# Optimization experiments

Hardware: AMD Instinct MI355X
Metric: run time of the kernel (lower is better)

The kernel has to match this reference:

```python
import jax, jax.numpy as jnp
import numpy as np

# split_shape from init_kwargs: list of (K, L) = (num slices, slice length)
SPLITS = [(1, 400), (60, 256), (36, 256)]
D_MODEL = 512
BATCH = 2048
EPS = 1e-5  # torch LayerNorm default


def setup_inputs() -> dict:
    key = jax.random.key(0)
    n = len(SPLITS)
    ks = jax.random.split(key, 1 + n)
    total_dim = sum(k * l for k, l in SPLITS)
    inp = {"x": jax.random.normal(ks[0], (BATCH, total_dim), jnp.float32)}
    for i, (k, l) in enumerate(SPLITS):
        # orthogonal-ish init approximated by scaled normal; LN affine = identity
        inp[f"W{i}"] = jax.random.normal(ks[1 + i], (l, D_MODEL), jnp.float32) / np.sqrt(l).astype(np.float32)
        inp[f"b{i}"] = jnp.zeros((D_MODEL,), jnp.float32)
        inp[f"g{i}"] = jnp.ones((D_MODEL,), jnp.float32)
        inp[f"be{i}"] = jnp.zeros((D_MODEL,), jnp.float32)
    return inp


def _fc_block(xs, W, b, g, be):
    # xs: [B, K, L] -> Linear + ReLU + LayerNorm -> [B, K, D]
    h = jax.nn.relu(jnp.einsum('bkl,ld->bkd', xs, W) + b)
    mu = jnp.mean(h, axis=-1, keepdims=True)
    var = jnp.var(h, axis=-1, keepdims=True)
    return (h - mu) * jax.lax.rsqrt(var + EPS) * g + be


def reference(x, W0, b0, g0, be0, W1, b1, g1, be1, W2, b2, g2, be2):
    params = [(W0, b0, g0, be0), (W1, b1, g1, be1), (W2, b2, g2, be2)]
    outs = []
    start = 0
    B = x.shape[0]
    for (k, l), (W, b, g, be) in zip(SPLITS, params):
        # the torch loop over j (K slices) is one batched GEMM after a reshape
        seg = x[:, start:start + k * l].reshape(B, k, l)
        outs.append(_fc_block(seg, W, b, g, be))
        start += k * l
    # torch.stack(x1, 1) over all K_i slices == concat of per-split [B,K_i,D]
    return jnp.concatenate(outs, axis=1)  # [B, sum(K_i)=97, D]
```

## Files before the change

### kernel.cpp

```cpp
#include <hip/hip_runtime.h>

#define TOTAL_DIM 24976
#define N_ROWS    97
#define D_MODEL   512
#define EPSLN     1e-5f

#define NB0 32
#define NB1 1920
#define NB2 1152

#define WT_TOTAL 475136
#define WT_BYTES (WT_TOTAL * 2)

#define SMEM_FUSED 61952

typedef __attribute__((ext_vector_type(8))) short frag8;
typedef __attribute__((ext_vector_type(4))) float frag4;

__device__ __forceinline__ unsigned short f2b(float f) {
  unsigned u = __float_as_uint(f);
  u = u + 0x7fffu + ((u >> 16) & 1u);
  return (unsigned short)(u >> 16);
}

__device__ __forceinline__ unsigned cvt2bf(float lo, float hi) {
  unsigned r;
  asm("v_cvt_pk_bf16_f32 %0, %1, %2" : "=v"(r) : "v"(lo), "v"(hi));
  return r;
}

__global__ void __launch_bounds__(256) prep_wt(const float* __restrict__ W0,
                                               const float* __restrict__ W1,
                                               const float* __restrict__ W2,
                                               unsigned short* __restrict__ wt) {
  int i = blockIdx.x * 256 + threadIdx.x;
  if (i >= WT_TOTAL / 4) return;
  const float* W; int L, NSTEP, u;
  if (i < 53248)      { W = W0; L = 400; NSTEP = 13; u = i; }
  else if (i < 86016) { W = W1; L = 256; NSTEP = 8;  u = i - 53248; }
  else                { W = W2; L = 256; NSTEP = 8;  u = i - 86016; }
  int j4 = u & 1;
  int l  = (u >> 1) & 63;
  int fi = u >> 7;
  int t  = fi % NSTEP;
  int nt = fi / NSTEP;
  int n  = nt * 16 + (l & 15);
  int k0 = t * 32 + (l >> 4) * 8 + j4 * 4;
  float v[4];
#pragma unroll
  for (int j = 0; j < 4; ++j) {
    int k = k0 + j;
    v[j] = (k < L) ? W[k * 512 + n] : 0.f;
  }
  unsigned lo = (unsigned)f2b(v[0]) | ((unsigned)f2b(v[1]) << 16);
  unsigned hi = (unsigned)f2b(v[2]) | ((unsigned)f2b(v[3]) << 16);
  ((uint2*)wt)[i] = make_uint2(lo, hi);
}

template <int S>
__device__ __forceinline__ void run_split(
    int blk, char* smem,
    const float* __restrict__ x, const unsigned short* __restrict__ wt,
    const float* __restrict__ bias, const float* __restrict__ gam,
    const float* __restrict__ bet, float* __restrict__ out) {
  constexpr int L     = (S == 0) ? 400 : 256;
  constexpr int KP    = (S == 0) ? 416 : 256;
  constexpr int NSTEP = KP / 32;
  constexpr int START = (S == 0) ? 0 : (S == 1) ? 400 : 15760;
  constexpr int KK    = (S == 0) ? 1 : (S == 1) ? 60 : 36;
  constexpr int OFF   = (S == 0) ? 0 : (S == 1) ? 1 : 61;
  constexpr int WTO   = (S == 0) ? 0 : (S == 1) ? 212992 : 344064;
  constexpr int RS    = KP * 2;
  constexpr bool SWZ  = (S != 0);

  unsigned short* A = (unsigned short*)smem;
  float* red  = (float*)(smem + 64 * RS);
  float* stat = (float*)(smem + 64 * RS + 8192);

  const int tid  = threadIdx.x;
  const int lane = tid & 63, w = tid >> 6;
  const int q = lane >> 4, c = lane & 15;
  const int m_base = blk * 64;

  const unsigned short* bp0 = wt + WTO + (2 * w) * (NSTEP * 512) + lane * 8;
  const unsigned short* bp1 = bp0 + NSTEP * 512;

  frag8 bc0 = *(const frag8*)bp0;
  frag8 bc1 = *(const frag8*)bp1;

  {
    int r = tid >> 4, ch = tid & 15;
    int m = m_base + r;
    int bb = m / KK, jj = m - bb * KK;
    const float* rp = x + (size_t)bb * TOTAL_DIM + START + (size_t)jj * L;
    constexpr int NPASS = (S == 0) ? 7 : 4;
#pragma unroll
    for (int p = 0; p < NPASS; ++p) {
      int c4 = ch + p * 16;
      if (S == 0 && c4 >= 104) continue;
      float4 v;
      if (S == 0 && c4 >= 100) {
        v.x = 0.f; v.y = 0.f; v.z = 0.f; v.w = 0.f;
      } else {
        v = *(const float4*)(rp + c4 * 4);
      }
      unsigned lo = cvt2bf(v.x, v.y), hi = cvt2bf(v.z, v.w);
      int off = c4 * 8;
      if (SWZ) off ^= ((r & 7) << 4);
      *(uint2*)((char*)A + r * RS + off) = make_uint2(lo, hi);
    }
  }

  frag4 acc[4][2];
#pragma unroll
  for (int mt = 0; mt < 4; ++mt)
#pragma unroll
    for (int nt = 0; nt < 2; ++nt) {
      frag4 z = {0.f, 0.f, 0.f, 0.f};
      acc[mt][nt] = z;
    }

  __syncthreads();

  const int sw = SWZ ? ((c & 7) << 4) : 0;

#pragma unroll
  for (int t = 0; t < NSTEP; ++t) {
    frag8 bn0, bn1;
    const bool pre = (t + 1 < NSTEP);
    if (pre) {
      bn0 = *(const frag8*)(bp0 + (t + 1) * 512);
      bn1 = *(const frag8*)(bp1 + (t + 1) * 512);
    }
    frag8 af[4];
    const int off = (t * 64 + q * 16) ^ sw;
#pragma unroll
    for (int mt = 0; mt < 4; ++mt)
      af[mt] = *(const frag8*)((char*)A + (mt * 16 + c) * RS + off);
#pragma unroll
    for (int mt = 0; mt < 4; ++mt) {
      acc[mt][0] = __builtin_amdgcn_mfma_f32_16x16x32_bf16(af[mt], bc0, acc[mt][0], 0, 0, 0);
      acc[mt][1] = __builtin_amdgcn_mfma_f32_16x16x32_bf16(af[mt], bc1, acc[mt][1], 0, 0, 0);
    }
    if (pre) { bc0 = bn0; bc1 = bn1; }
  }

  const int colbase = w * 32 + c;
  float bv[2], gv[2], ev[2];
#pragma unroll
  for (int nt = 0; nt < 2; ++nt) {
    int col = colbase + nt * 16;
    bv[nt] = bias[col];
    gv[nt] = gam[col];
    ev[nt] = bet[col];
  }

#pragma unroll
  for (int mt = 0; mt < 4; ++mt) {
    float s[4] = {0.f, 0.f, 0.f, 0.f}, s2[4] = {0.f, 0.f, 0.f, 0.f};
#pragma unroll
    for (int nt = 0; nt < 2; ++nt)
#pragma unroll
      for (int r = 0; r < 4; ++r) {
        float h = acc[mt][nt][r] + bv[nt];
        h = fmaxf(h, 0.f);
        acc[mt][nt][r] = h;
        s[r] += h;
        s2[r] += h * h;
      }
#pragma unroll
    for (int r = 0; r < 4; ++r) {
      float a = s[r], b2 = s2[r];
#pragma unroll
      for (int msk = 1; msk < 16; msk <<= 1) {
        a += __shfl_xor(a, msk, 64);
        b2 += __shfl_xor(b2, msk, 64);
      }
      if (c == 0) {
        int row = mt * 16 + q * 4 + r;
        red[(w * 64 + row) * 2 + 0] = a;
        red[(w * 64 + row) * 2 + 1] = b2;
      }
    }
  }
  __syncthreads();
  if (tid < 64) {
    float s = 0.f, s2 = 0.f;
#pragma unroll
    for (int ww = 0; ww < 16; ++ww) {
      s  += red[(ww * 64 + tid) * 2 + 0];
      s2 += red[(ww * 64 + tid) * 2 + 1];
    }
    float mu  = s * (1.f / 512.f);
    float var = s2 * (1.f / 512.f) - mu * mu;
    stat[tid * 2 + 0] = mu;
    stat[tid * 2 + 1] = rsqrtf(var + EPSLN);
  }
  __syncthreads();

#pragma unroll
  for (int mt = 0; mt < 4; ++mt)
#pragma unroll
    for (int r = 0; r < 4; ++r) {
      int row = mt * 16 + q * 4 + r;
      float mu = stat[row * 2 + 0], sc = stat[row * 2 + 1];
      int m = m_base + row;
      int bb = m / KK, jj = m - bb * KK;
      size_t orow = (size_t)bb * N_ROWS + OFF + jj;
      float* op = out + orow * D_MODEL + colbase;
#pragma unroll
      for (int nt = 0; nt < 2; ++nt)
        op[nt * 16] = (acc[mt][nt][r] - mu) * sc * gv[nt] + ev[nt];
    }
}

__global__ void __launch_bounds__(1024, 4) fused_kernel(
    const float* __restrict__ x, const unsigned short* __restrict__ wt,
    const float* __restrict__ b0, const float* __restrict__ g0, const float* __restrict__ e0,
    const float* __restrict__ b1, const float* __restrict__ g1, const float* __restrict__ e1,
    const float* __restrict__ b2, const float* __restrict__ g2, const float* __restrict__ e2,
    float* __restrict__ out) {
  extern __shared__ char smem[];
  int bid = blockIdx.x;
  if (bid < NB0)
    run_split<0>(bid, smem, x, wt, b0, g0, e0, out);
  else if (bid < NB0 + NB1)
    run_split<1>(bid - NB0, smem, x, wt, b1, g1, e1, out);
  else
    run_split<2>(bid - NB0 - NB1, smem, x, wt, b2, g2, e2, out);
}

template <int S>
__global__ void __launch_bounds__(256) fallback_split(
    const float* __restrict__ x, const float* __restrict__ W,
    const float* __restrict__ bias, const float* __restrict__ gam,
    const float* __restrict__ bet, float* __restrict__ out) {
  constexpr int L     = (S == 0) ? 400 : 256;
  constexpr int START = (S == 0) ? 0 : (S == 1) ? 400 : 15760;
  constexpr int KK    = (S == 0) ? 1 : (S == 1) ? 60 : 36;
  constexpr int OFF   = (S == 0) ? 0 : (S == 1) ? 1 : 61;

  __shared__ float xs[400];
  __shared__ float rs[4], rs2[4];

  int m = blockIdx.x;
  int bb = m / KK, jj = m - bb * KK;
  const float* xp = x + (size_t)bb * TOTAL_DIM + START + jj * L;
  for (int k = threadIdx.x; k < L; k += 256) xs[k] = xp[k];
  __syncthreads();

  float h[2];
#pragma unroll
  for (int i = 0; i < 2; ++i) {
    int col = threadIdx.x + i * 256;
    float acc = 0.f;
    for (int k = 0; k < L; ++k) acc += xs[k] * W[k * 512 + col];
    h[i] = fmaxf(acc + bias[col], 0.f);
  }

  float s = h[0] + h[1], s2 = h[0] * h[0] + h[1] * h[1];
#pragma unroll
  for (int msk = 1; msk < 64; msk <<= 1) {
    s  += __shfl_xor(s, msk, 64);
    s2 += __shfl_xor(s2, msk, 64);
  }
  int wave = threadIdx.x >> 6, lane = threadIdx.x & 63;
  if (lane == 0) { rs[wave] = s; rs2[wave] = s2; }
  __syncthreads();
  s  = rs[0] + rs[1] + rs[2] + rs[3];
  s2 = rs2[0] + rs2[1] + rs2[2] + rs2[3];
  float mu  = s * (1.f / 512.f);
  float var = s2 * (1.f / 512.f) - mu * mu;
  float sc  = rsqrtf(var + EPSLN);

  float* op = out + ((size_t)bb * N_ROWS + OFF + jj) * D_MODEL;
#pragma unroll
  for (int i = 0; i < 2; ++i) {
    int col = threadIdx.x + i * 256;
    op[col] = (h[i] - mu) * sc * gam[col] + bet[col];
  }
}

extern "C" void kernel_launch(void* const* d_in, const int* in_sizes, int n_in,
                              void* d_out, int out_size, void* d_ws, size_t ws_size,
                              hipStream_t stream) {
  const float* x  = (const float*)d_in[0];
  const float* W0 = (const float*)d_in[1];
  const float* b0 = (const float*)d_in[2];
  const float* g0 = (const float*)d_in[3];
  const float* e0 = (const float*)d_in[4];
  const float* W1 = (const float*)d_in[5];
  const float* b1 = (const float*)d_in[6];
  const float* g1 = (const float*)d_in[7];
  const float* e1 = (const float*)d_in[8];
  const float* W2 = (const float*)d_in[9];
  const float* b2 = (const float*)d_in[10];
  const float* g2 = (const float*)d_in[11];
  const float* e2 = (const float*)d_in[12];
  float* out = (float*)d_out;

  if (ws_size >= (size_t)WT_BYTES) {
    unsigned short* wt = (unsigned short*)d_ws;
    prep_wt<<<464, 256, 0, stream>>>(W0, W1, W2, wt);
    fused_kernel<<<NB0 + NB1 + NB2, 1024, SMEM_FUSED, stream>>>(
        x, wt, b0, g0, e0, b1, g1, e1, b2, g2, e2, out);
  } else {
    fallback_split<0><<<2048,   256, 0, stream>>>(x, W0, b0, g0, e0, out);
    fallback_split<1><<<122880, 256, 0, stream>>>(x, W1, b1, g1, e1, out);
    fallback_split<2><<<73728,  256, 0, stream>>>(x, W2, b2, g2, e2, out);
  }
}
```

Baseline: 681.0 us.

## Switch to persistent 256-block kernel with register-resident weights and prefetched A tiles

Replaces the one-tile-per-block grid with 256 persistent blocks that each process 24 tiles of 32 rows. Each wave keeps its full weight slice in registers across tiles, and the next tile's x rows are prefetched into registers while the current tile's MFMAs run. Split 0 tiles are folded into the first 64 blocks of the split-2 range. The aim is to cut repeated weight loads and block launch overhead and to hide global latency. The cost is higher register pressure, a smaller M tile per block, and a fixed tile mapping hardcoded to this batch size.

```diff
diff --git a/kernel.cpp b/kernel.cpp
--- a/kernel.cpp
+++ b/kernel.cpp
@@ -5,14 +5,10 @@
 #define D_MODEL   512
 #define EPSLN     1e-5f
 
-#define NB0 32
-#define NB1 1920
-#define NB2 1152
-
 #define WT_TOTAL 475136
 #define WT_BYTES (WT_TOTAL * 2)
 
-#define SMEM_FUSED 61952
+#define SMEM_FUSED 30976
 
 typedef __attribute__((ext_vector_type(8))) short frag8;
 typedef __attribute__((ext_vector_type(4))) float frag4;
@@ -57,106 +53,13 @@
   ((uint2*)wt)[i] = make_uint2(lo, hi);
 }
 
-template <int S>
-__device__ __forceinline__ void run_split(
-    int blk, char* smem,
-    const float* __restrict__ x, const unsigned short* __restrict__ wt,
-    const float* __restrict__ bias, const float* __restrict__ gam,
-    const float* __restrict__ bet, float* __restrict__ out) {
-  constexpr int L     = (S == 0) ? 400 : 256;
-  constexpr int KP    = (S == 0) ? 416 : 256;
-  constexpr int NSTEP = KP / 32;
-  constexpr int START = (S == 0) ? 0 : (S == 1) ? 400 : 15760;
-  constexpr int KK    = (S == 0) ? 1 : (S == 1) ? 60 : 36;
-  constexpr int OFF   = (S == 0) ? 0 : (S == 1) ? 1 : 61;
-  constexpr int WTO   = (S == 0) ? 0 : (S == 1) ? 212992 : 344064;
-  constexpr int RS    = KP * 2;
-  constexpr bool SWZ  = (S != 0);
-
-  unsigned short* A = (unsigned short*)smem;
-  float* red  = (float*)(smem + 64 * RS);
-  float* stat = (float*)(smem + 64 * RS + 8192);
-
-  const int tid  = threadIdx.x;
-  const int lane = tid & 63, w = tid >> 6;
-  const int q = lane >> 4, c = lane & 15;
-  const int m_base = blk * 64;
-
-  const unsigned short* bp0 = wt + WTO + (2 * w) * (NSTEP * 512) + lane * 8;
-  const unsigned short* bp1 = bp0 + NSTEP * 512;
-
-  frag8 bc0 = *(const frag8*)bp0;
-  frag8 bc1 = *(const frag8*)bp1;
-
-  {
-    int r = tid >> 4, ch = tid & 15;
-    int m = m_base + r;
-    int bb = m / KK, jj = m - bb * KK;
-    const float* rp = x + (size_t)bb * TOTAL_DIM + START + (size_t)jj * L;
-    constexpr int NPASS = (S == 0) ? 7 : 4;
-#pragma unroll
-    for (int p = 0; p < NPASS; ++p) {
-      int c4 = ch + p * 16;
-      if (S == 0 && c4 >= 104) continue;
-      float4 v;
-      if (S == 0 && c4 >= 100) {
-        v.x = 0.f; v.y = 0.f; v.z = 0.f; v.w = 0.f;
-      } else {
-        v = *(const float4*)(rp + c4 * 4);
-      }
-      unsigned lo = cvt2bf(v.x, v.y), hi = cvt2bf(v.z, v.w);
-      int off = c4 * 8;
-      if (SWZ) off ^= ((r & 7) << 4);
-      *(uint2*)((char*)A + r * RS + off) = make_uint2(lo, hi);
-    }
-  }
-
-  frag4 acc[4][2];
-#pragma unroll
-  for (int mt = 0; mt < 4; ++mt)
-#pragma unroll
-    for (int nt = 0; nt < 2; ++nt) {
-      frag4 z = {0.f, 0.f, 0.f, 0.f};
-      acc[mt][nt] = z;
-    }
-
-  __syncthreads();
-
-  const int sw = SWZ ? ((c & 7) << 4) : 0;
-
-#pragma unroll
-  for (int t = 0; t < NSTEP; ++t) {
-    frag8 bn0, bn1;
-    const bool pre = (t + 1 < NSTEP);
-    if (pre) {
-      bn0 = *(const frag8*)(bp0 + (t + 1) * 512);
-      bn1 = *(const frag8*)(bp1 + (t + 1) * 512);
-    }
-    frag8 af[4];
-    const int off = (t * 64 + q * 16) ^ sw;
-#pragma unroll
-    for (int mt = 0; mt < 4; ++mt)
-      af[mt] = *(const frag8*)((char*)A + (mt * 16 + c) * RS + off);
-#pragma unroll
-    for (int mt = 0; mt < 4; ++mt) {
-      acc[mt][0] = __builtin_amdgcn_mfma_f32_16x16x32_bf16(af[mt], bc0, acc[mt][0], 0, 0, 0);
-      acc[mt][1] = __builtin_amdgcn_mfma_f32_16x16x32_bf16(af[mt], bc1, acc[mt][1], 0, 0, 0);
-    }
-    if (pre) { bc0 = bn0; bc1 = bn1; }
-  }
-
-  const int colbase = w * 32 + c;
-  float bv[2], gv[2], ev[2];
-#pragma unroll
-  for (int nt = 0; nt < 2; ++nt) {
-    int col = colbase + nt * 16;
-    bv[nt] = bias[col];
-    gv[nt] = gam[col];
-    ev[nt] = bet[col];
-  }
-
-#pragma unroll
-  for (int mt = 0; mt < 4; ++mt) {
+template <int KK, int OFF>
+__device__ __forceinline__ void epilogue32(
+    frag4 (&acc)[2][2], int m_base, int w, int q, int c, int tid, int colbase,
+    const float (&bv)[2], const float (&gv)[2], const float (&ev)[2],
+    float* red, float* stat, float* __restrict__ out) {
+#pragma unroll
+  for (int mt = 0; mt < 2; ++mt) {
     float s[4] = {0.f, 0.f, 0.f, 0.f}, s2[4] = {0.f, 0.f, 0.f, 0.f};
 #pragma unroll
     for (int nt = 0; nt < 2; ++nt)
@@ -178,18 +81,18 @@
       }
       if (c == 0) {
         int row = mt * 16 + q * 4 + r;
-        red[(w * 64 + row) * 2 + 0] = a;
-        red[(w * 64 + row) * 2 + 1] = b2;
+        red[(w * 32 + row) * 2 + 0] = a;
+        red[(w * 32 + row) * 2 + 1] = b2;
       }
     }
   }
   __syncthreads();
-  if (tid < 64) {
+  if (tid < 32) {
     float s = 0.f, s2 = 0.f;
 #pragma unroll
     for (int ww = 0; ww < 16; ++ww) {
-      s  += red[(ww * 64 + tid) * 2 + 0];
-      s2 += red[(ww * 64 + tid) * 2 + 1];
+      s  += red[(ww * 32 + tid) * 2 + 0];
+      s2 += red[(ww * 32 + tid) * 2 + 1];
     }
     float mu  = s * (1.f / 512.f);
     float var = s2 * (1.f / 512.f) - mu * mu;
@@ -197,9 +100,8 @@
     stat[tid * 2 + 1] = rsqrtf(var + EPSLN);
   }
   __syncthreads();
-
-#pragma unroll
-  for (int mt = 0; mt < 4; ++mt)
+#pragma unroll
+  for (int mt = 0; mt < 2; ++mt)
 #pragma unroll
     for (int r = 0; r < 4; ++r) {
       int row = mt * 16 + q * 4 + r;
@@ -214,6 +116,179 @@
     }
 }
 
+template <int S>
+__device__ __forceinline__ void run_persistent(
+    int tile0, int ntiles, char* smem,
+    const float* __restrict__ x, const unsigned short* __restrict__ wt,
+    const float* __restrict__ bias, const float* __restrict__ gam,
+    const float* __restrict__ bet, float* __restrict__ out) {
+  constexpr int L     = 256, NSTEP = 8;
+  constexpr int START = (S == 1) ? 400 : 15760;
+  constexpr int KK    = (S == 1) ? 60 : 36;
+  constexpr int OFF   = (S == 1) ? 1 : 61;
+  constexpr int WTO   = (S == 1) ? 212992 : 344064;
+  constexpr int RS    = 512;
+
+  unsigned short* A = (unsigned short*)smem;
+  float* red  = (float*)(smem + 16384);
+  float* stat = (float*)(smem + 20480);
+
+  const int tid = threadIdx.x, lane = tid & 63, w = tid >> 6;
+  const int q = lane >> 4, c = lane & 15;
+  const int sr = tid >> 5, sch = tid & 31;
+  const int swr = (sr & 7) << 4;
+  const int sw  = (c & 7) << 4;
+
+  frag8 bc[NSTEP][2];
+#pragma unroll
+  for (int nt = 0; nt < 2; ++nt)
+#pragma unroll
+    for (int t = 0; t < NSTEP; ++t)
+      bc[t][nt] = *(const frag8*)(wt + WTO + ((2 * w + nt) * NSTEP + t) * 512 + lane * 8);
+
+  const int colbase = w * 32 + c;
+  float bv[2], gv[2], ev[2];
+#pragma unroll
+  for (int nt = 0; nt < 2; ++nt) {
+    bv[nt] = bias[colbase + nt * 16];
+    gv[nt] = gam[colbase + nt * 16];
+    ev[nt] = bet[colbase + nt * 16];
+  }
+
+  float4 st0, st1;
+  {
+    int m = tile0 * 32 + sr;
+    int bb = m / KK, jj = m - bb * KK;
+    const float* rp = x + (size_t)bb * TOTAL_DIM + START + (size_t)jj * L + sch * 4;
+    st0 = *(const float4*)rp;
+    st1 = *(const float4*)(rp + 128);
+  }
+  {
+    *(uint2*)((char*)A + sr * RS + ((sch * 8) ^ swr)) =
+        make_uint2(cvt2bf(st0.x, st0.y), cvt2bf(st0.z, st0.w));
+    *(uint2*)((char*)A + sr * RS + ((sch * 8 + 256) ^ swr)) =
+        make_uint2(cvt2bf(st1.x, st1.y), cvt2bf(st1.z, st1.w));
+  }
+  __syncthreads();
+
+  for (int i = 0; i < ntiles; ++i) {
+    const int m_base = (tile0 + i) * 32;
+    const bool more = (i + 1 < ntiles);
+    if (more) {
+      int m = m_base + 32 + sr;
+      int bb = m / KK, jj = m - bb * KK;
+      const float* rp = x + (size_t)bb * TOTAL_DIM + START + (size_t)jj * L + sch * 4;
+      st0 = *(const float4*)rp;
+      st1 = *(const float4*)(rp + 128);
+    }
+
+    frag4 acc[2][2];
+#pragma unroll
+    for (int mt = 0; mt < 2; ++mt)
+#pragma unroll
+      for (int nt = 0; nt < 2; ++nt) {
+        frag4 z = {0.f, 0.f, 0.f, 0.f};
+        acc[mt][nt] = z;
+      }
+
+#pragma unroll
+    for (int t = 0; t < NSTEP; ++t) {
+      const int off = (t * 64 + q * 16) ^ sw;
+      frag8 a0 = *(const frag8*)((char*)A + (c) * RS + off);
+      frag8 a1 = *(const frag8*)((char*)A + (16 + c) * RS + off);
+      acc[0][0] = __builtin_amdgcn_mfma_f32_16x16x32_bf16(a0, bc[t][0], acc[0][0], 0, 0, 0);
+      acc[0][1] = __builtin_amdgcn_mfma_f32_16x16x32_bf16(a0, bc[t][1], acc[0][1], 0, 0, 0);
+      acc[1][0] = __builtin_amdgcn_mfma_f32_16x16x32_bf16(a1, bc[t][0], acc[1][0], 0, 0, 0);
+      acc[1][1] = __builtin_amdgcn_mfma_f32_16x16x32_bf16(a1, bc[t][1], acc[1][1], 0, 0, 0);
+    }
+    __syncthreads();
+    if (more) {
+      *(uint2*)((char*)A + sr * RS + ((sch * 8) ^ swr)) =
+          make_uint2(cvt2bf(st0.x, st0.y), cvt2bf(st0.z, st0.w));
+      *(uint2*)((char*)A + sr * RS + ((sch * 8 + 256) ^ swr)) =
+          make_uint2(cvt2bf(st1.x, st1.y), cvt2bf(st1.z, st1.w));
+    }
+    epilogue32<KK, OFF>(acc, m_base, w, q, c, tid, colbase, bv, gv, ev,
+                        red, stat, out);
+  }
+}
+
+__device__ __forceinline__ void run_s0(
+    int tile, char* smem,
+    const float* __restrict__ x, const unsigned short* __restrict__ wt,
+    const float* __restrict__ bias, const float* __restrict__ gam,
+    const float* __restrict__ bet, float* __restrict__ out) {
+  constexpr int L = 400, NSTEP = 13, RS = 832;
+
+  unsigned short* A = (unsigned short*)smem;
+  float* red  = (float*)(smem + 26624);
+  float* stat = (float*)(smem + 30720);
+
+  const int tid = threadIdx.x, lane = tid & 63, w = tid >> 6;
+  const int q = lane >> 4, c = lane & 15;
+  const int sr = tid >> 5, sch = tid & 31;
+
+  const unsigned short* bp0 = wt + (2 * w) * (NSTEP * 512) + lane * 8;
+  const unsigned short* bp1 = bp0 + NSTEP * 512;
+  frag8 bc0 = *(const frag8*)bp0;
+  frag8 bc1 = *(const frag8*)bp1;
+
+  {
+    int m = tile * 32 + sr;
+    const float* rp = x + (size_t)m * TOTAL_DIM;
+#pragma unroll
+    for (int p = 0; p < 4; ++p) {
+      int c4 = sch + p * 32;
+      if (c4 >= 104) continue;
+      float4 v;
+      if (c4 >= 100) { v.x = 0.f; v.y = 0.f; v.z = 0.f; v.w = 0.f; }
+      else           { v = *(const float4*)(rp + c4 * 4); }
+      *(uint2*)((char*)A + sr * RS + c4 * 8) =
+          make_uint2(cvt2bf(v.x, v.y), cvt2bf(v.z, v.w));
+    }
+  }
+
+  const int colbase = w * 32 + c;
+  float bv[2], gv[2], ev[2];
+#pragma unroll
+  for (int nt = 0; nt < 2; ++nt) {
+    bv[nt] = bias[colbase + nt * 16];
+    gv[nt] = gam[colbase + nt * 16];
+    ev[nt] = bet[colbase + nt * 16];
+  }
+
+  frag4 acc[2][2];
+#pragma unroll
+  for (int mt = 0; mt < 2; ++mt)
+#pragma unroll
+    for (int nt = 0; nt < 2; ++nt) {
+      frag4 z = {0.f, 0.f, 0.f, 0.f};
+      acc[mt][nt] = z;
+    }
+  __syncthreads();
+
+#pragma unroll
+  for (int t = 0; t < NSTEP; ++t) {
+    frag8 bn0, bn1;
+    const bool pre = (t + 1 < NSTEP);
+    if (pre) {
+      bn0 = *(const frag8*)(bp0 + (t + 1) * 512);
+      bn1 = *(const frag8*)(bp1 + (t + 1) * 512);
+    }
+    const int off = t * 64 + q * 16;
+    frag8 a0 = *(const frag8*)((char*)A + (c) * RS + off);
+    frag8 a1 = *(const frag8*)((char*)A + (16 + c) * RS + off);
+    acc[0][0] = __builtin_amdgcn_mfma_f32_16x16x32_bf16(a0, bc0, acc[0][0], 0, 0, 0);
+    acc[0][1] = __builtin_amdgcn_mfma_f32_16x16x32_bf16(a0, bc1, acc[0][1], 0, 0, 0);
+    acc[1][0] = __builtin_amdgcn_mfma_f32_16x16x32_bf16(a1, bc0, acc[1][0], 0, 0, 0);
+    acc[1][1] = __builtin_amdgcn_mfma_f32_16x16x32_bf16(a1, bc1, acc[1][1], 0, 0, 0);
+    if (pre) { bc0 = bn0; bc1 = bn1; }
+  }
+  __syncthreads();
+  epilogue32<1, 0>(acc, tile * 32, w, q, c, tid, colbase, bv, gv, ev,
+                   red, stat, out);
+}
+
 __global__ void __launch_bounds__(1024, 4) fused_kernel(
     const float* __restrict__ x, const unsigned short* __restrict__ wt,
     const float* __restrict__ b0, const float* __restrict__ g0, const float* __restrict__ e0,
@@ -221,13 +296,14 @@
     const float* __restrict__ b2, const float* __restrict__ g2, const float* __restrict__ e2,
     float* __restrict__ out) {
   extern __shared__ char smem[];
-  int bid = blockIdx.x;
-  if (bid < NB0)
-    run_split<0>(bid, smem, x, wt, b0, g0, e0, out);
-  else if (bid < NB0 + NB1)
-    run_split<1>(bid - NB0, smem, x, wt, b1, g1, e1, out);
-  else
-    run_split<2>(bid - NB0 - NB1, smem, x, wt, b2, g2, e2, out);
+  int b = blockIdx.x;
+  if (b < 160) {
+    run_persistent<1>(b * 24, 24, smem, x, wt, b1, g1, e1, out);
+  } else {
+    int s2b = b - 160;
+    if (s2b < 64) run_s0(s2b, smem, x, wt, b0, g0, e0, out);
+    run_persistent<2>(s2b * 24, 24, smem, x, wt, b2, g2, e2, out);
+  }
 }
 
 template <int S>
@@ -302,7 +378,7 @@
   if (ws_size >= (size_t)WT_BYTES) {
     unsigned short* wt = (unsigned short*)d_ws;
     prep_wt<<<464, 256, 0, stream>>>(W0, W1, W2, wt);
-    fused_kernel<<<NB0 + NB1 + NB2, 1024, SMEM_FUSED, stream>>>(
+    fused_kernel<<<256, 1024, SMEM_FUSED, stream>>>(
         x, wt, b0, g0, e0, b1, g1, e1, b2, g2, e2, out);
   } else {
     fallback_split<0><<<2048,   256, 0, stream>>>(x, W0, b0, g0, e0, out);
```

Result: slower. 771.5 us (+13.3%).

## Shrink fused block tile to 16 rows with 512 threads per block

Applied to the files above, without the earlier changes.

Each block now processes 16 rows instead of 64, with 8 waves each computing 4 column tiles from one shared A fragment, and launches four times as many blocks with less shared memory. The aim is higher occupancy and finer-grained scheduling to hide memory latency in this bandwidth-bound GEMM+LayerNorm. In exchange, weight fragments are re-read four times as often per output row and the register prefetch of B fragments is removed.

```diff
diff --git a/kernel.cpp b/kernel.cpp
--- a/kernel.cpp
+++ b/kernel.cpp
@@ -5,14 +5,14 @@
 #define D_MODEL   512
 #define EPSLN     1e-5f
 
-#define NB0 32
-#define NB1 1920
-#define NB2 1152
+#define NB0 128
+#define NB1 7680
+#define NB2 4608
 
 #define WT_TOTAL 475136
 #define WT_BYTES (WT_TOTAL * 2)
 
-#define SMEM_FUSED 61952
+#define SMEM_FUSED 14464
 
 typedef __attribute__((ext_vector_type(8))) short frag8;
 typedef __attribute__((ext_vector_type(4))) float frag4;
@@ -58,7 +58,7 @@
 }
 
 template <int S>
-__device__ __forceinline__ void run_split(
+__device__ __forceinline__ void run16(
     int blk, char* smem,
     const float* __restrict__ x, const unsigned short* __restrict__ wt,
     const float* __restrict__ bias, const float* __restrict__ gam,
@@ -74,147 +74,127 @@
   constexpr bool SWZ  = (S != 0);
 
   unsigned short* A = (unsigned short*)smem;
-  float* red  = (float*)(smem + 64 * RS);
-  float* stat = (float*)(smem + 64 * RS + 8192);
-
-  const int tid  = threadIdx.x;
-  const int lane = tid & 63, w = tid >> 6;
+  float* red  = (float*)(smem + 16 * RS);
+  float* stat = (float*)(smem + 16 * RS + 1024);
+
+  const int tid = threadIdx.x, lane = tid & 63, w = tid >> 6;
   const int q = lane >> 4, c = lane & 15;
-  const int m_base = blk * 64;
-
-  const unsigned short* bp0 = wt + WTO + (2 * w) * (NSTEP * 512) + lane * 8;
-  const unsigned short* bp1 = bp0 + NSTEP * 512;
-
-  frag8 bc0 = *(const frag8*)bp0;
-  frag8 bc1 = *(const frag8*)bp1;
+  const int m_base = blk * 16;
 
   {
-    int r = tid >> 4, ch = tid & 15;
-    int m = m_base + r;
+    int sr = tid >> 5, sch = tid & 31;
+    int m = m_base + sr;
     int bb = m / KK, jj = m - bb * KK;
     const float* rp = x + (size_t)bb * TOTAL_DIM + START + (size_t)jj * L;
-    constexpr int NPASS = (S == 0) ? 7 : 4;
-#pragma unroll
-    for (int p = 0; p < NPASS; ++p) {
-      int c4 = ch + p * 16;
-      if (S == 0 && c4 >= 104) continue;
-      float4 v;
-      if (S == 0 && c4 >= 100) {
-        v.x = 0.f; v.y = 0.f; v.z = 0.f; v.w = 0.f;
-      } else {
-        v = *(const float4*)(rp + c4 * 4);
+    if (S == 0) {
+#pragma unroll
+      for (int p = 0; p < 4; ++p) {
+        int c4 = sch + p * 32;
+        if (c4 >= 104) continue;
+        float4 v;
+        if (c4 >= 100) { v.x = 0.f; v.y = 0.f; v.z = 0.f; v.w = 0.f; }
+        else           { v = *(const float4*)(rp + c4 * 4); }
+        *(uint2*)((char*)A + sr * RS + c4 * 8) =
+            make_uint2(cvt2bf(v.x, v.y), cvt2bf(v.z, v.w));
       }
-      unsigned lo = cvt2bf(v.x, v.y), hi = cvt2bf(v.z, v.w);
-      int off = c4 * 8;
-      if (SWZ) off ^= ((r & 7) << 4);
-      *(uint2*)((char*)A + r * RS + off) = make_uint2(lo, hi);
-    }
-  }
-
-  frag4 acc[4][2];
-#pragma unroll
-  for (int mt = 0; mt < 4; ++mt)
-#pragma unroll
-    for (int nt = 0; nt < 2; ++nt) {
-      frag4 z = {0.f, 0.f, 0.f, 0.f};
-      acc[mt][nt] = z;
-    }
+    } else {
+      const int swr = (sr & 7) << 4;
+      float4 v0 = *(const float4*)(rp + sch * 4);
+      float4 v1 = *(const float4*)(rp + sch * 4 + 128);
+      *(uint2*)((char*)A + sr * RS + ((sch * 8) ^ swr)) =
+          make_uint2(cvt2bf(v0.x, v0.y), cvt2bf(v0.z, v0.w));
+      *(uint2*)((char*)A + sr * RS + ((sch * 8 + 256) ^ swr)) =
+          make_uint2(cvt2bf(v1.x, v1.y), cvt2bf(v1.z, v1.w));
+    }
+  }
+
+  frag4 acc[4];
+#pragma unroll
+  for (int nt = 0; nt < 4; ++nt) {
+    frag4 z = {0.f, 0.f, 0.f, 0.f};
+    acc[nt] = z;
+  }
 
   __syncthreads();
 
   const int sw = SWZ ? ((c & 7) << 4) : 0;
+  const unsigned short* bbase = wt + WTO + (w * 4) * (NSTEP * 512) + lane * 8;
 
 #pragma unroll
   for (int t = 0; t < NSTEP; ++t) {
-    frag8 bn0, bn1;
-    const bool pre = (t + 1 < NSTEP);
-    if (pre) {
-      bn0 = *(const frag8*)(bp0 + (t + 1) * 512);
-      bn1 = *(const frag8*)(bp1 + (t + 1) * 512);
-    }
-    frag8 af[4];
-    const int off = (t * 64 + q * 16) ^ sw;
-#pragma unroll
-    for (int mt = 0; mt < 4; ++mt)
-      af[mt] = *(const frag8*)((char*)A + (mt * 16 + c) * RS + off);
-#pragma unroll
-    for (int mt = 0; mt < 4; ++mt) {
-      acc[mt][0] = __builtin_amdgcn_mfma_f32_16x16x32_bf16(af[mt], bc0, acc[mt][0], 0, 0, 0);
-      acc[mt][1] = __builtin_amdgcn_mfma_f32_16x16x32_bf16(af[mt], bc1, acc[mt][1], 0, 0, 0);
-    }
-    if (pre) { bc0 = bn0; bc1 = bn1; }
-  }
-
-  const int colbase = w * 32 + c;
-  float bv[2], gv[2], ev[2];
-#pragma unroll
-  for (int nt = 0; nt < 2; ++nt) {
+    frag8 af = *(const frag8*)((char*)A + c * RS + ((t * 64 + q * 16) ^ sw));
+#pragma unroll
+    for (int nt = 0; nt < 4; ++nt) {
+      frag8 bf = *(const frag8*)(bbase + (nt * NSTEP + t) * 512);
+      acc[nt] = __builtin_amdgcn_mfma_f32_16x16x32_bf16(af, bf, acc[nt], 0, 0, 0);
+    }
+  }
+
+  const int colbase = w * 64 + c;
+  float bv[4], gv[4], ev[4];
+#pragma unroll
+  for (int nt = 0; nt < 4; ++nt) {
     int col = colbase + nt * 16;
     bv[nt] = bias[col];
     gv[nt] = gam[col];
     ev[nt] = bet[col];
   }
 
-#pragma unroll
-  for (int mt = 0; mt < 4; ++mt) {
-    float s[4] = {0.f, 0.f, 0.f, 0.f}, s2[4] = {0.f, 0.f, 0.f, 0.f};
-#pragma unroll
-    for (int nt = 0; nt < 2; ++nt)
-#pragma unroll
-      for (int r = 0; r < 4; ++r) {
-        float h = acc[mt][nt][r] + bv[nt];
-        h = fmaxf(h, 0.f);
-        acc[mt][nt][r] = h;
-        s[r] += h;
-        s2[r] += h * h;
-      }
+  float s[4] = {0.f, 0.f, 0.f, 0.f}, s2[4] = {0.f, 0.f, 0.f, 0.f};
+#pragma unroll
+  for (int nt = 0; nt < 4; ++nt)
 #pragma unroll
     for (int r = 0; r < 4; ++r) {
-      float a = s[r], b2 = s2[r];
-#pragma unroll
-      for (int msk = 1; msk < 16; msk <<= 1) {
-        a += __shfl_xor(a, msk, 64);
-        b2 += __shfl_xor(b2, msk, 64);
-      }
-      if (c == 0) {
-        int row = mt * 16 + q * 4 + r;
-        red[(w * 64 + row) * 2 + 0] = a;
-        red[(w * 64 + row) * 2 + 1] = b2;
-      }
-    }
-  }
-  __syncthreads();
-  if (tid < 64) {
-    float s = 0.f, s2 = 0.f;
-#pragma unroll
-    for (int ww = 0; ww < 16; ++ww) {
-      s  += red[(ww * 64 + tid) * 2 + 0];
-      s2 += red[(ww * 64 + tid) * 2 + 1];
-    }
-    float mu  = s * (1.f / 512.f);
-    float var = s2 * (1.f / 512.f) - mu * mu;
+      float h = acc[nt][r] + bv[nt];
+      h = fmaxf(h, 0.f);
+      acc[nt][r] = h;
+      s[r] += h;
+      s2[r] += h * h;
+    }
+#pragma unroll
+  for (int r = 0; r < 4; ++r) {
+    float a = s[r], b2 = s2[r];
+#pragma unroll
+    for (int msk = 1; msk < 16; msk <<= 1) {
+      a += __shfl_xor(a, msk, 64);
+      b2 += __shfl_xor(b2, msk, 64);
+    }
+    if (c == 0) {
+      int row = q * 4 + r;
+      red[(row * 8 + w) * 2 + 0] = a;
+      red[(row * 8 + w) * 2 + 1] = b2;
+    }
+  }
+  __syncthreads();
+  if (tid < 16) {
+    float s0 = 0.f, s20 = 0.f;
+#pragma unroll
+    for (int ww = 0; ww < 8; ++ww) {
+      s0  += red[(tid * 8 + ww) * 2 + 0];
+      s20 += red[(tid * 8 + ww) * 2 + 1];
+    }
+    float mu  = s0 * (1.f / 512.f);
+    float var = s20 * (1.f / 512.f) - mu * mu;
     stat[tid * 2 + 0] = mu;
     stat[tid * 2 + 1] = rsqrtf(var + EPSLN);
   }
   __syncthreads();
 
 #pragma unroll
-  for (int mt = 0; mt < 4; ++mt)
-#pragma unroll
-    for (int r = 0; r < 4; ++r) {
-      int row = mt * 16 + q * 4 + r;
-      float mu = stat[row * 2 + 0], sc = stat[row * 2 + 1];
-      int m = m_base + row;
-      int bb = m / KK, jj = m - bb * KK;
-      size_t orow = (size_t)bb * N_ROWS + OFF + jj;
-      float* op = out + orow * D_MODEL + colbase;
-#pragma unroll
-      for (int nt = 0; nt < 2; ++nt)
-        op[nt * 16] = (acc[mt][nt][r] - mu) * sc * gv[nt] + ev[nt];
-    }
-}
-
-__global__ void __launch_bounds__(1024, 4) fused_kernel(
+  for (int r = 0; r < 4; ++r) {
+    int row = q * 4 + r;
+    float mu = stat[row * 2 + 0], sc = stat[row * 2 + 1];
+    int m = m_base + row;
+    int bb = m / KK, jj = m - bb * KK;
+    size_t orow = (size_t)bb * N_ROWS + OFF + jj;
+    float* op = out + orow * D_MODEL + colbase;
+#pragma unroll
+    for (int nt = 0; nt < 4; ++nt)
+      op[nt * 16] = (acc[nt][r] - mu) * sc * gv[nt] + ev[nt];
+  }
+}
+
+__global__ void __launch_bounds__(512, 8) fused_kernel(
     const float* __restrict__ x, const unsigned short* __restrict__ wt,
     const float* __restrict__ b0, const float* __restrict__ g0, const float* __restrict__ e0,
     const float* __restrict__ b1, const float* __restrict__ g1, const float* __restrict__ e1,
@@ -223,11 +203,11 @@
   extern __shared__ char smem[];
   int bid = blockIdx.x;
   if (bid < NB0)
-    run_split<0>(bid, smem, x, wt, b0, g0, e0, out);
+    run16<0>(bid, smem, x, wt, b0, g0, e0, out);
   else if (bid < NB0 + NB1)
-    run_split<1>(bid - NB0, smem, x, wt, b1, g1, e1, out);
+    run16<1>(bid - NB0, smem, x, wt, b1, g1, e1, out);
   else
-    run_split<2>(bid - NB0 - NB1, smem, x, wt, b2, g2, e2, out);
+    run16<2>(bid - NB0 - NB1, smem, x, wt, b2, g2, e2, out);
 }
 
 template <int S>
@@ -302,7 +282,7 @@
   if (ws_size >= (size_t)WT_BYTES) {
     unsigned short* wt = (unsigned short*)d_ws;
     prep_wt<<<464, 256, 0, stream>>>(W0, W1, W2, wt);
-    fused_kernel<<<NB0 + NB1 + NB2, 1024, SMEM_FUSED, stream>>>(
+    fused_kernel<<<NB0 + NB1 + NB2, 512, SMEM_FUSED, stream>>>(
         x, wt, b0, g0, e0, b1, g1, e1, b2, g2, e2, out);
   } else {
     fallback_split<0><<<2048,   256, 0, stream>>>(x, W0, b0, g0, e0, out);
```

Measured after the change: 639.1 us. 1.07x faster.
